# Optimization experiments

Measured on AMD Instinct MI355X. Metric: run time of the kernel, lower is better.

Reference implementation:

```python
import jax, jax.numpy as jnp
import numpy as np

B, Q, H, W, C = 2, 8192, 64, 64, 64
C9 = C * 9
EPS = 1e-6


def _mlp(x, params):
    # gelu MLP, no activation on last layer (matches repo mlp)
    for Wm, b in params[:-1]:
        x = jax.nn.gelu(x @ Wm + b)
    Wl, bl = params[-1]
    return x @ Wl + bl


def _make_coord(h, w):
    # pixel-center coords in (-1,1); channel 0 = row dim, channel 1 = col dim
    hs = -1.0 + (2.0 * jnp.arange(h, dtype=jnp.float32) + 1.0) / h
    ws = -1.0 + (2.0 * jnp.arange(w, dtype=jnp.float32) + 1.0) / w
    return jnp.stack(jnp.meshgrid(hs, ws, indexing='ij'), axis=0)  # (2,h,w)


def _nearest_gather(feat, coord):
    # F.grid_sample(mode='nearest', align_corners=False) on a (B,1,q,2) grid.
    # feat (B,C,H,W); coord (B,q,2) with [...,0] indexing H, [...,1] indexing W
    h, w = feat.shape[-2], feat.shape[-1]
    ih = jnp.clip(jnp.round((coord[..., 0] + 1.0) * h / 2.0 - 0.5), 0, h - 1).astype(jnp.int32)
    iw = jnp.clip(jnp.round((coord[..., 1] + 1.0) * w / 2.0 - 0.5), 0, w - 1).astype(jnp.int32)
    return jax.vmap(lambda f, a, b: f[:, a, b].T)(feat, ih, iw)  # (B,q,C)


def _unfold3(feat):
    # F.unfold(feat, 3, padding=1).view(B, C*9, H, W): channel-major, kernel row-major
    b, c, h, w = feat.shape
    p = jnp.pad(feat, ((0, 0), (0, 0), (1, 1), (1, 1)))
    patches = jnp.stack([p[:, :, i:i + h, j:j + w] for i in range(3) for j in range(3)], axis=2)
    return patches.reshape(b, c * 9, h, w)


def _forward(inp, coord, scale, enc_w, enc_b, iw0, ib0, iw1, ib1, iw2, ib2,
             sw0, sb0, sw1, sb1, ww0, wb0, ww1, wb1):
    # encoder (stand-in conv3x3, 3 -> C feature channels)
    feat = jax.lax.conv_general_dilated(inp, enc_w, (1, 1), 'SAME',
                                        dimension_numbers=('NCHW', 'OIHW', 'NCHW'))
    feat = feat + enc_b[None, :, None, None]
    feat = _unfold3(feat)  # (B, C*9, H, W)
    bsz, cf, h, w = feat.shape
    fcoord = jnp.broadcast_to(_make_coord(h, w)[None], (bsz, 2, h, w))
    dims = jnp.array([h, w], dtype=feat.dtype)

    tx = (h - 1) / (1.0 - scale[:, 0, 0])  # (B,)
    ty = (w - 1) / (1.0 - scale[:, 0, 1])
    rx, ry = 1.0 / tx, 1.0 / ty
    scale_tok = scale * dims  # (B,q,2)

    imnet_p = [(iw0, ib0), (iw1, ib1), (iw2, ib2)]
    score_p = [(sw0, sb0), (sw1, sb1)]
    weight_p = [(ww0, wb0), (ww1, wb1)]

    preds = []
    for vx in (-1, 1):
        for vy in (-1, 1):
            shift = jnp.stack([vx * rx + EPS, vy * ry + EPS], axis=-1)[:, None, :]  # (B,1,2)
            c = jnp.clip(coord + shift, -1.0 + 1e-6, 1.0 - 1e-6)
            value = _nearest_gather(feat, c)      # (B,q,C*9)
            coord_k = _nearest_gather(fcoord, c)  # (B,q,2)
            rel = (coord - coord_k) * dims        # (B,q,2)
            score = _mlp(rel, score_p)            # (B,q,1) -> broadcast over 3
            mlp_in = jnp.concatenate([rel, scale_tok], axis=-1)  # (B,q,4)
            wmat = _mlp(mlp_in, imnet_p).reshape(bsz, -1, cf, 3)  # (B,q,C*9,3)
            preds.append(jnp.einsum('bqc,bqck->bqk', value, wmat) + score)
    stacked = jnp.stack(preds, axis=-1)  # (B,q,3,4)
    return _mlp(stacked, weight_p)[..., 0]  # (B,q,3)


def setup_inputs() -> dict:
    key = jax.random.key(0)
    ks = jax.random.split(key, 16)
    f32 = jnp.float32

    def wi(k, shape, fan_in):
        return jax.random.normal(k, shape, f32) / np.float32(np.sqrt(fan_in))

    return {
        'inp': jax.random.normal(ks[0], (B, 3, H, W), f32),
        'coord': jax.random.uniform(ks[1], (B, Q, 2), f32, -1.0 + 1e-4, 1.0 - 1e-4),
        'scale': jax.random.uniform(ks[2], (B, Q, 2), f32, 0.01, 0.05),
        'enc_w': wi(ks[3], (C, 3, 3, 3), 27),
        'enc_b': jnp.zeros((C,), f32),
        'iw0': wi(ks[4], (4, 256), 4), 'ib0': jnp.zeros((256,), f32),
        'iw1': wi(ks[5], (256, 256), 256), 'ib1': jnp.zeros((256,), f32),
        'iw2': wi(ks[6], (256, C9 * 3), 256), 'ib2': jnp.zeros((C9 * 3,), f32),
        'sw0': wi(ks[7], (2, 256), 2), 'sb0': jnp.zeros((256,), f32),
        'sw1': wi(ks[8], (256, 1), 256), 'sb1': jnp.zeros((1,), f32),
        'ww0': wi(ks[9], (4, 256), 4), 'wb0': jnp.zeros((256,), f32),
        'ww1': wi(ks[10], (256, 1), 256), 'wb1': jnp.zeros((1,), f32),
    }


def reference(inp, coord, scale, enc_w, enc_b, iw0, ib0, iw1, ib1, iw2, ib2,
              sw0, sb0, sw1, sb1, ww0, wb0, ww1, wb1):
    return _forward(inp, coord, scale, enc_w, enc_b, iw0, ib0, iw1, ib1, iw2, ib2,
                    sw0, sb0, sw1, sb1, ww0, wb0, ww1, wb1)
```

## Files before the change

### kernel.cpp

```cpp
#include <hip/hip_runtime.h>

#define QN 8192
#define CCH 64
#define NROW 65536
#define MR 64
#define NBLK (NROW / MR)
#define H0S 264

typedef _Float16 f16x8 __attribute__((ext_vector_type(8)));
typedef _Float16 f16x4 __attribute__((ext_vector_type(4)));
typedef float f32x4 __attribute__((ext_vector_type(4)));

__device__ __forceinline__ float gelu_f(float x) {
    float x2 = x * x;
    float tt = fmaf(0.044715f, x2, 1.0f);
    float e = __expf(1.5957691216f * x * tt);
    float r = __builtin_amdgcn_rcpf(1.0f + e);
    return x - x * r;
}

__global__ __launch_bounds__(256) void k_pre(const float* __restrict__ inp,
                                             const float* __restrict__ ew,
                                             const float* __restrict__ eb,
                                             const float* __restrict__ coord,
                                             const float* __restrict__ scale,
                                             const float* __restrict__ sw0,
                                             const float* __restrict__ sb0,
                                             const float* __restrict__ sw1,
                                             const float* __restrict__ sb1,
                                             const float* __restrict__ iw1,
                                             const float* __restrict__ iw2,
                                             const float* __restrict__ ib2,
                                             float* __restrict__ featpad,
                                             float4* __restrict__ mlp_in,
                                             int2* __restrict__ ihiw,
                                             float* __restrict__ scoreg,
                                             _Float16* __restrict__ w1tp,
                                             _Float16* __restrict__ w2tp,
                                             float* __restrict__ b2p) {
    const int bb = blockIdx.x;
    const int tt0 = threadIdx.x;
    if (bb < 2178) {
        __shared__ float s_ew[1728];
        for (int i = tt0; i < 1728; i += 256) s_ew[i] = ew[i];
        __syncthreads();
        int idx = bb * 256 + tt0;
        const int total = 2 * 66 * 66 * CCH;
        if (idx >= total) return;
        int o = idx & 63; int pix = idx >> 6;
        int xx = pix % 66; int t2 = pix / 66;
        int yy = t2 % 66;  int b = t2 / 66;
        int y = yy - 1, x = xx - 1;
        float acc = 0.0f;
        if (y >= 0 && y < 64 && x >= 0 && x < 64) {
            acc = eb[o];
            for (int i = 0; i < 3; ++i) {
                const float* ip = inp + ((b * 3 + i) * 64) * 64;
                const float* wp = s_ew + (o * 3 + i) * 9;
                #pragma unroll
                for (int ky = 0; ky < 3; ++ky) {
                    int sy = y + ky - 1;
                    if (sy < 0 || sy > 63) continue;
                    #pragma unroll
                    for (int kx = 0; kx < 3; ++kx) {
                        int sx = x + kx - 1;
                        if (sx < 0 || sx > 63) continue;
                        acc += ip[sy * 64 + sx] * wp[ky * 3 + kx];
                    }
                }
            }
        }
        featpad[idx] = acc;
    } else if (bb < 2434) {
        int row = (bb - 2178) * 256 + tt0;
        int v = row & 3;
        int bq = row >> 2;
        int b = bq >> 13;
        float c0 = coord[bq * 2 + 0], c1 = coord[bq * 2 + 1];
        float s0 = scale[bq * 2 + 0], s1 = scale[bq * 2 + 1];
        float s00 = scale[(b * QN) * 2 + 0];
        float s01 = scale[(b * QN) * 2 + 1];
        float rx = (1.0f - s00) / 63.0f;
        float ry = (1.0f - s01) / 63.0f;
        float vx = (v & 2) ? 1.0f : -1.0f;
        float vy = (v & 1) ? 1.0f : -1.0f;
        float cc0 = c0 + vx * rx + 1e-6f;
        float cc1 = c1 + vy * ry + 1e-6f;
        cc0 = fminf(fmaxf(cc0, -1.0f + 1e-6f), 1.0f - 1e-6f);
        cc1 = fminf(fmaxf(cc1, -1.0f + 1e-6f), 1.0f - 1e-6f);
        int ih = (int)rintf((cc0 + 1.0f) * 32.0f - 0.5f);
        int iw = (int)rintf((cc1 + 1.0f) * 32.0f - 0.5f);
        ih = min(max(ih, 0), 63);
        iw = min(max(iw, 0), 63);
        float ck0 = (2.0f * (float)ih + 1.0f) / 64.0f - 1.0f;
        float ck1 = (2.0f * (float)iw + 1.0f) / 64.0f - 1.0f;
        float rel0 = (c0 - ck0) * 64.0f;
        float rel1 = (c1 - ck1) * 64.0f;
        mlp_in[row] = make_float4(rel0, rel1, s0 * 64.0f, s1 * 64.0f);
        ihiw[row] = make_int2(ih, iw);
        float sc = sb1[0];
        #pragma unroll 4
        for (int t2 = 0; t2 < 256; ++t2) {
            float h = gelu_f(fmaf(rel0, sw0[t2], fmaf(rel1, sw0[256 + t2], sb0[t2])));
            sc = fmaf(h, sw1[t2], sc);
        }
        scoreg[row] = sc;
    } else {
        int idx = (bb - 2434) * 256 + tt0;
        if (idx < 442368) {
            int j = idx & 7, ln = (idx >> 3) & 63, kf = (idx >> 9) & 7, tl = idx >> 12;
            int np = tl * 16 + (ln & 15);
            int kk = kf * 32 + (ln >> 4) * 8 + j;
            int k_out = np / 576;
            int rem = np - 576 * k_out;
            int tap = rem >> 6, cch = rem & 63;
            int n = (cch * 9 + tap) * 3 + k_out;
            w2tp[idx] = (_Float16)iw2[kk * 1728 + n];
            if (kf == 0 && j == 0 && (ln >> 4) == 0) b2p[np] = ib2[n];
        } else {
            int i2 = idx - 442368;
            int j = i2 & 7, ln = (i2 >> 3) & 63, kf = (i2 >> 9) & 7, ct = i2 >> 12;
            int col = ct * 16 + (ln & 15);
            int kk = kf * 32 + (ln >> 4) * 8 + j;
            w1tp[i2] = (_Float16)iw1[kk * 256 + col];
        }
    }
}

__global__ __launch_bounds__(256, 2) void k_fused(const float* __restrict__ featpad,
                                                  const float4* __restrict__ mlp_in,
                                                  const int2* __restrict__ ihiw,
                                                  const float* __restrict__ iw0,
                                                  const float* __restrict__ ib0,
                                                  const _Float16* __restrict__ w1tp,
                                                  const float* __restrict__ ib1,
                                                  const _Float16* __restrict__ w2tp,
                                                  const float* __restrict__ b2p,
                                                  const float* __restrict__ scoreg,
                                                  const float* __restrict__ ww0,
                                                  const float* __restrict__ wb0,
                                                  const float* __restrict__ ww1,
                                                  const float* __restrict__ wb1,
                                                  float* __restrict__ out) {
    __shared__ __align__(16) char pool[576 * 64 * 2];
    _Float16* s_h0   = (_Float16*)pool;
    _Float16* s_valT = (_Float16*)pool;
    __shared__ float4 s_min[MR];
    __shared__ int    s_base[MR];
    __shared__ int    s_dtab[9];
    __shared__ float  s_pred[MR][3];
    __shared__ float  s_score[MR];
    __shared__ float  s_wred[48][4];

    const int t = threadIdx.x;
    const int wave = t >> 6, lane = t & 63, quad = lane >> 4, l15 = lane & 15;
    const int rowbase = blockIdx.x * MR;

    if (t < MR) {
        int row = rowbase + t;
        s_min[t] = mlp_in[row];
        s_score[t] = scoreg[row];
        int b = row >> 15;
        int2 p = ihiw[row];
        s_base[t] = ((b * 66 + p.x) * 66 + p.y) * 64;
    }
    if (t < 9) { int di = t / 3; s_dtab[t] = (di * 66 + (t - 3 * di)) * 64; }
    if (t < MR * 3) s_pred[t / 3][t % 3] = 0.0f;
    __syncthreads();

    {
        float w0 = iw0[t], w1 = iw0[256 + t], w2 = iw0[512 + t], w3 = iw0[768 + t];
        float bb = ib0[t];
        #pragma unroll 4
        for (int r = 0; r < MR; ++r) {
            float4 m = s_min[r];
            s_h0[r * H0S + t] =
                (_Float16)gelu_f(fmaf(m.x, w0, fmaf(m.y, w1, fmaf(m.z, w2, fmaf(m.w, w3, bb)))));
        }
    }
    __syncthreads();

    f16x8 a[4][8];
    #pragma unroll
    for (int rt = 0; rt < 4; ++rt)
        #pragma unroll
        for (int kf = 0; kf < 8; ++kf)
            a[rt][kf] = *(const f16x8*)(s_h0 + (rt * 16 + l15) * H0S + kf * 32 + quad * 8);
    __syncthreads();

    #pragma unroll 1
    for (int c = 0; c < 4; ++c) {
        int ct = wave * 4 + c;
        f16x8 bf[8];
        #pragma unroll
        for (int kf = 0; kf < 8; ++kf)
            bf[kf] = *(const f16x8*)(w1tp + ((ct * 8 + kf) * 64 + lane) * 8);
        f32x4 acc[4] = {{0.f,0.f,0.f,0.f},{0.f,0.f,0.f,0.f},{0.f,0.f,0.f,0.f},{0.f,0.f,0.f,0.f}};
        #pragma unroll
        for (int kf = 0; kf < 8; ++kf)
            #pragma unroll
            for (int rt = 0; rt < 4; ++rt)
                acc[rt] = __builtin_amdgcn_mfma_f32_16x16x32_f16(a[rt][kf], bf[kf], acc[rt], 0, 0, 0);
        int col = ct * 16 + l15;
        float bias = ib1[col];
        #pragma unroll
        for (int rt = 0; rt < 4; ++rt)
            #pragma unroll
            for (int reg = 0; reg < 4; ++reg)
                s_h0[(rt * 16 + quad * 4 + reg) * H0S + col] = (_Float16)gelu_f(acc[rt][reg] + bias);
    }
    __syncthreads();

    #pragma unroll
    for (int rt = 0; rt < 4; ++rt)
        #pragma unroll
        for (int kf = 0; kf < 8; ++kf)
            a[rt][kf] = *(const f16x8*)(s_h0 + (rt * 16 + l15) * H0S + kf * 32 + quad * 8);
    __syncthreads();

    #pragma unroll 1
    for (int pp = 0; pp < 36; ++pp) {
        int c4 = wave + pp * 4;
        int row = lane;
        int tap = c4 >> 4;
        int cch0 = (c4 & 15) << 2;
        const float4 v = *(const float4*)(featpad + s_base[row] + s_dtab[tap] + cch0);
        int cfp = c4 << 2;
        s_valT[(cfp + 0) * 64 + (row ^ (((cfp + 0) & 7) << 3))] = (_Float16)v.x;
        s_valT[(cfp + 1) * 64 + (row ^ (((cfp + 1) & 7) << 3))] = (_Float16)v.y;
        s_valT[(cfp + 2) * 64 + (row ^ (((cfp + 2) & 7) << 3))] = (_Float16)v.z;
        s_valT[(cfp + 3) * 64 + (row ^ (((cfp + 3) & 7) << 3))] = (_Float16)v.w;
    }
    __syncthreads();

    const int tbase = wave * 27;
    const int kt0 = tbase / 36;
    int bsplit = (kt0 + 1) * 36 - tbase; if (bsplit > 27) bsplit = 27;
    const int ktB = (kt0 + 1 < 3) ? kt0 + 1 : 2;
    const int swz = (l15 & 7) << 3;

    float pA[4][4], pB[4][4];
    #pragma unroll
    for (int rt = 0; rt < 4; ++rt)
        #pragma unroll
        for (int rg = 0; rg < 4; ++rg) { pA[rt][rg] = 0.f; pB[rt][rg] = 0.f; }

    f16x8 bf[8];
    float bv;
    {
        const _Float16* wp = w2tp + (size_t)(tbase * 8) * 512 + lane * 8;
        #pragma unroll
        for (int kf = 0; kf < 8; ++kf) bf[kf] = *(const f16x8*)(wp + kf * 512);
        bv = b2p[tbase * 16 + l15];
    }
    #pragma unroll 1
    for (int i = 0; i < 27; ++i) {
        f32x4 acc[4] = {{0.f,0.f,0.f,0.f},{0.f,0.f,0.f,0.f},{0.f,0.f,0.f,0.f},{0.f,0.f,0.f,0.f}};
        #pragma unroll
        for (int kf = 0; kf < 8; ++kf)
            #pragma unroll
            for (int rt = 0; rt < 4; ++rt)
                acc[rt] = __builtin_amdgcn_mfma_f32_16x16x32_f16(a[rt][kf], bf[kf], acc[rt], 0, 0, 0);
        float bvc = bv;
        int ti = tbase + i;
        if (i < 26) {
            const _Float16* wp = w2tp + (size_t)((ti + 1) * 8) * 512 + lane * 8;
            #pragma unroll
            for (int kf = 0; kf < 8; ++kf) bf[kf] = *(const f16x8*)(wp + kf * 512);
            bv = b2p[(ti + 1) * 16 + l15];
        }
        int cf36 = ti - (ti / 36) * 36;
        const _Float16* vbase = s_valT + (cf36 * 16 + l15) * 64;
        if (i < bsplit) {
            #pragma unroll
            for (int rt = 0; rt < 4; ++rt) {
                f16x4 vv = *(const f16x4*)(vbase + ((rt * 16 + quad * 4) ^ swz));
                #pragma unroll
                for (int rg = 0; rg < 4; ++rg) {
                    float w = (float)vv[rg];
                    pA[rt][rg] = fmaf(acc[rt][rg], w, fmaf(bvc, w, pA[rt][rg]));
                }
            }
        } else {
            #pragma unroll
            for (int rt = 0; rt < 4; ++rt) {
                f16x4 vv = *(const f16x4*)(vbase + ((rt * 16 + quad * 4) ^ swz));
                #pragma unroll
                for (int rg = 0; rg < 4; ++rg) {
                    float w = (float)vv[rg];
                    pB[rt][rg] = fmaf(acc[rt][rg], w, fmaf(bvc, w, pB[rt][rg]));
                }
            }
        }
    }

    #pragma unroll
    for (int rt = 0; rt < 4; ++rt)
        #pragma unroll
        for (int rg = 0; rg < 4; ++rg) {
            float aA = pA[rt][rg], aB = pB[rt][rg];
            #pragma unroll
            for (int m = 1; m < 16; m <<= 1) {
                aA += __shfl_xor(aA, m, 64);
                aB += __shfl_xor(aB, m, 64);
            }
            if (l15 == 0) {
                int rr = rt * 16 + quad * 4 + rg;
                atomicAdd(&s_pred[rr][kt0], aA);
                atomicAdd(&s_pred[rr][ktB], aB);
            }
        }
    __syncthreads();

    if (t < 192) {
        int o = t >> 2, sub = t & 3;
        int bql = o / 3, k = o - 3 * bql;
        float x0 = s_pred[bql * 4 + 0][k] + s_score[bql * 4 + 0];
        float x1 = s_pred[bql * 4 + 1][k] + s_score[bql * 4 + 1];
        float x2 = s_pred[bql * 4 + 2][k] + s_score[bql * 4 + 2];
        float x3 = s_pred[bql * 4 + 3][k] + s_score[bql * 4 + 3];
        float acc = 0.0f;
        int j0 = sub * 64;
        #pragma unroll 4
        for (int j = j0; j < j0 + 64; ++j) {
            float h = gelu_f(fmaf(x0, ww0[j], fmaf(x1, ww0[256 + j],
                          fmaf(x2, ww0[512 + j], fmaf(x3, ww0[768 + j], wb0[j])))));
            acc = fmaf(h, ww1[j], acc);
        }
        s_wred[o][sub] = acc;
    }
    __syncthreads();
    if (t < 48) {
        int bql = t / 3, k = t - 3 * bql;
        float r2 = s_wred[t][0] + s_wred[t][1] + s_wred[t][2] + s_wred[t][3] + wb1[0];
        out[(blockIdx.x * 16 + bql) * 3 + k] = r2;
    }
}

extern "C" void kernel_launch(void* const* d_in, const int* in_sizes, int n_in,
                              void* d_out, int out_size, void* d_ws, size_t ws_size,
                              hipStream_t stream) {
    const float* inp   = (const float*)d_in[0];
    const float* coord = (const float*)d_in[1];
    const float* scale = (const float*)d_in[2];
    const float* ew    = (const float*)d_in[3];
    const float* eb    = (const float*)d_in[4];
    const float* iw0   = (const float*)d_in[5];
    const float* ib0   = (const float*)d_in[6];
    const float* iw1   = (const float*)d_in[7];
    const float* ib1   = (const float*)d_in[8];
    const float* iw2   = (const float*)d_in[9];
    const float* ib2   = (const float*)d_in[10];
    const float* sw0   = (const float*)d_in[11];
    const float* sb0   = (const float*)d_in[12];
    const float* sw1   = (const float*)d_in[13];
    const float* sb1   = (const float*)d_in[14];
    const float* ww0   = (const float*)d_in[15];
    const float* wb0   = (const float*)d_in[16];
    const float* ww1   = (const float*)d_in[17];
    const float* wb1   = (const float*)d_in[18];
    float* out = (float*)d_out;

    char* ws = (char*)d_ws;
    float*     featpad = (float*)(ws + 0);
    float4*    mlp_in  = (float4*)(ws + 2230272);
    int2*      ihiw    = (int2*)(ws + 3278848);
    float*     scoreg  = (float*)(ws + 3803136);
    _Float16*  w1tp    = (_Float16*)(ws + 4065280);
    _Float16*  w2tp    = (_Float16*)(ws + 4196352);
    float*     b2p     = (float*)(ws + 5081088);

    k_pre<<<dim3(4418), dim3(256), 0, stream>>>(inp, ew, eb, coord, scale,
                                                sw0, sb0, sw1, sb1, iw1, iw2, ib2,
                                                featpad, mlp_in, ihiw, scoreg,
                                                w1tp, w2tp, b2p);
    k_fused<<<dim3(NBLK), dim3(256), 0, stream>>>(featpad, mlp_in, ihiw,
                                                  iw0, ib0, w1tp, ib1, w2tp, b2p,
                                                  scoreg, ww0, wb0, ww1, wb1, out);
}
```

Baseline: 249.8 us.

## Split weight prefetch into halves, merge accumulators, rework feature gather swizzle

The second-layer weight fragments are now double-buffered in two halves (bfX/bfY) instead of a full 8-fragment prefetch, which cuts live vector registers. The two partial-sum arrays are merged into one, with an in-loop reduction and flush at the tap boundary. The feature-gather loop is remapped so each lane loads a contiguous channel quad per row-tap pair, with a new 4-bit XOR swizzle on the transposed LDS tile. The aim is lower register pressure and fewer LDS bank conflicts, at the cost of more exposed weight-load latency and an extra shuffle reduction inside the loop.

```diff
diff --git a/kernel.cpp b/kernel.cpp
--- a/kernel.cpp
+++ b/kernel.cpp
@@ -218,97 +218,101 @@
             a[rt][kf] = *(const f16x8*)(s_h0 + (rt * 16 + l15) * H0S + kf * 32 + quad * 8);
     __syncthreads();
 
+    const int tbase = wave * 27;
+    f16x8 bfX[4], bfY[4];
+    {
+        const _Float16* wp = w2tp + (size_t)(tbase * 8) * 512 + lane * 8;
+        #pragma unroll
+        for (int kf = 0; kf < 4; ++kf) bfX[kf] = *(const f16x8*)(wp + kf * 512);
+    }
+
     #pragma unroll 1
-    for (int pp = 0; pp < 36; ++pp) {
-        int c4 = wave + pp * 4;
-        int row = lane;
-        int tap = c4 >> 4;
-        int cch0 = (c4 & 15) << 2;
-        const float4 v = *(const float4*)(featpad + s_base[row] + s_dtab[tap] + cch0);
-        int cfp = c4 << 2;
-        s_valT[(cfp + 0) * 64 + (row ^ (((cfp + 0) & 7) << 3))] = (_Float16)v.x;
-        s_valT[(cfp + 1) * 64 + (row ^ (((cfp + 1) & 7) << 3))] = (_Float16)v.y;
-        s_valT[(cfp + 2) * 64 + (row ^ (((cfp + 2) & 7) << 3))] = (_Float16)v.z;
-        s_valT[(cfp + 3) * 64 + (row ^ (((cfp + 3) & 7) << 3))] = (_Float16)v.w;
-    }
-    __syncthreads();
-
-    const int tbase = wave * 27;
+    for (int it = 0; it < 36; ++it) {
+        int p = (wave * 36 + it) * 4 + quad;
+        int r = (p * 7283) >> 16;
+        int tap = p - 9 * r;
+        const float4 v = *(const float4*)(featpad + s_base[r] + s_dtab[tap] + l15 * 4);
+        int cfp0 = tap * 64 + l15 * 4;
+        int g = (cfp0 & 15) << 2;
+        _Float16* wp = s_valT + cfp0 * 64 + (r ^ ((cfp0 & 12) << 2));
+        s_valT[(cfp0 + 0) * 64 + (r ^ (((cfp0 + 0) & 15) << 2))] = (_Float16)v.x;
+        s_valT[(cfp0 + 1) * 64 + (r ^ (((cfp0 + 1) & 15) << 2))] = (_Float16)v.y;
+        s_valT[(cfp0 + 2) * 64 + (r ^ (((cfp0 + 2) & 15) << 2))] = (_Float16)v.z;
+        s_valT[(cfp0 + 3) * 64 + (r ^ (((cfp0 + 3) & 15) << 2))] = (_Float16)v.w;
+        (void)g; (void)wp;
+    }
+    __syncthreads();
+
     const int kt0 = tbase / 36;
     int bsplit = (kt0 + 1) * 36 - tbase; if (bsplit > 27) bsplit = 27;
-    const int ktB = (kt0 + 1 < 3) ? kt0 + 1 : 2;
-    const int swz = (l15 & 7) << 3;
-
-    float pA[4][4], pB[4][4];
+    const int ktB = (tbase + 26) / 36;
+
+    float pA[4][4];
     #pragma unroll
     for (int rt = 0; rt < 4; ++rt)
         #pragma unroll
-        for (int rg = 0; rg < 4; ++rg) { pA[rt][rg] = 0.f; pB[rt][rg] = 0.f; }
-
-    f16x8 bf[8];
+        for (int rg = 0; rg < 4; ++rg) pA[rt][rg] = 0.f;
+
     float bv;
-    {
-        const _Float16* wp = w2tp + (size_t)(tbase * 8) * 512 + lane * 8;
-        #pragma unroll
-        for (int kf = 0; kf < 8; ++kf) bf[kf] = *(const f16x8*)(wp + kf * 512);
-        bv = b2p[tbase * 16 + l15];
-    }
     #pragma unroll 1
     for (int i = 0; i < 27; ++i) {
+        int ti = tbase + i;
+        {
+            const _Float16* wp = w2tp + (size_t)(ti * 8 + 4) * 512 + lane * 8;
+            #pragma unroll
+            for (int kf = 0; kf < 4; ++kf) bfY[kf] = *(const f16x8*)(wp + kf * 512);
+            bv = b2p[ti * 16 + l15];
+        }
         f32x4 acc[4] = {{0.f,0.f,0.f,0.f},{0.f,0.f,0.f,0.f},{0.f,0.f,0.f,0.f},{0.f,0.f,0.f,0.f}};
         #pragma unroll
-        for (int kf = 0; kf < 8; ++kf)
+        for (int kf = 0; kf < 4; ++kf)
             #pragma unroll
             for (int rt = 0; rt < 4; ++rt)
-                acc[rt] = __builtin_amdgcn_mfma_f32_16x16x32_f16(a[rt][kf], bf[kf], acc[rt], 0, 0, 0);
-        float bvc = bv;
-        int ti = tbase + i;
+                acc[rt] = __builtin_amdgcn_mfma_f32_16x16x32_f16(a[rt][kf], bfX[kf], acc[rt], 0, 0, 0);
         if (i < 26) {
             const _Float16* wp = w2tp + (size_t)((ti + 1) * 8) * 512 + lane * 8;
             #pragma unroll
-            for (int kf = 0; kf < 8; ++kf) bf[kf] = *(const f16x8*)(wp + kf * 512);
-            bv = b2p[(ti + 1) * 16 + l15];
-        }
+            for (int kf = 0; kf < 4; ++kf) bfX[kf] = *(const f16x8*)(wp + kf * 512);
+        }
+        #pragma unroll
+        for (int kf = 0; kf < 4; ++kf)
+            #pragma unroll
+            for (int rt = 0; rt < 4; ++rt)
+                acc[rt] = __builtin_amdgcn_mfma_f32_16x16x32_f16(a[rt][kf + 4], bfY[kf], acc[rt], 0, 0, 0);
         int cf36 = ti - (ti / 36) * 36;
-        const _Float16* vbase = s_valT + (cf36 * 16 + l15) * 64;
-        if (i < bsplit) {
-            #pragma unroll
-            for (int rt = 0; rt < 4; ++rt) {
-                f16x4 vv = *(const f16x4*)(vbase + ((rt * 16 + quad * 4) ^ swz));
+        int cfp = cf36 * 16 + l15;
+        int g = (cfp & 15) << 2;
+        const _Float16* vbase = s_valT + cfp * 64;
+        #pragma unroll
+        for (int rt = 0; rt < 4; ++rt) {
+            f16x4 vv = *(const f16x4*)(vbase + ((rt * 16 + quad * 4) ^ g));
+            #pragma unroll
+            for (int rg = 0; rg < 4; ++rg) {
+                float s = acc[rt][rg] + bv;
+                pA[rt][rg] = fmaf(s, (float)vv[rg], pA[rt][rg]);
+            }
+        }
+        if (i == bsplit - 1) {
+            #pragma unroll
+            for (int rt = 0; rt < 4; ++rt)
                 #pragma unroll
                 for (int rg = 0; rg < 4; ++rg) {
-                    float w = (float)vv[rg];
-                    pA[rt][rg] = fmaf(acc[rt][rg], w, fmaf(bvc, w, pA[rt][rg]));
+                    float x = pA[rt][rg];
+                    #pragma unroll
+                    for (int m = 1; m < 16; m <<= 1) x += __shfl_xor(x, m, 64);
+                    if (l15 == 0) atomicAdd(&s_pred[rt * 16 + quad * 4 + rg][kt0], x);
+                    pA[rt][rg] = 0.f;
                 }
-            }
-        } else {
-            #pragma unroll
-            for (int rt = 0; rt < 4; ++rt) {
-                f16x4 vv = *(const f16x4*)(vbase + ((rt * 16 + quad * 4) ^ swz));
-                #pragma unroll
-                for (int rg = 0; rg < 4; ++rg) {
-                    float w = (float)vv[rg];
-                    pB[rt][rg] = fmaf(acc[rt][rg], w, fmaf(bvc, w, pB[rt][rg]));
-                }
-            }
-        }
-    }
-
+        }
+    }
     #pragma unroll
     for (int rt = 0; rt < 4; ++rt)
         #pragma unroll
         for (int rg = 0; rg < 4; ++rg) {
-            float aA = pA[rt][rg], aB = pB[rt][rg];
-            #pragma unroll
-            for (int m = 1; m < 16; m <<= 1) {
-                aA += __shfl_xor(aA, m, 64);
-                aB += __shfl_xor(aB, m, 64);
-            }
-            if (l15 == 0) {
-                int rr = rt * 16 + quad * 4 + rg;
-                atomicAdd(&s_pred[rr][kt0], aA);
-                atomicAdd(&s_pred[rr][ktB], aB);
-            }
+            float x = pA[rt][rg];
+            #pragma unroll
+            for (int m = 1; m < 16; m <<= 1) x += __shfl_xor(x, m, 64);
+            if (l15 == 0) atomicAdd(&s_pred[rt * 16 + quad * 4 + rg][ktB], x);
         }
     __syncthreads();
 
```

After: 251.2 us. No clear change (+0.6%).
